# Optimization experiments

Hardware: AMD Instinct MI355X
Metric: run time of the kernel (lower is better)

The kernel has to match this reference:

```python
import jax, jax.numpy as jnp
import numpy as np

D = 1024      # embedding_dim
H = 16        # num_heads
DH = D // H   # head_dim
DFF = 4 * D
EPS = 1e-5


def setup_inputs() -> dict:
    key = jax.random.key(0)
    ks = jax.random.split(key, 10)
    B, T = 2, 2048
    s = 0.02
    return {
        "x": jax.random.normal(ks[0], (B, T, D), dtype=jnp.float32),
        "Wq": jax.random.normal(ks[1], (H, D, DH), dtype=jnp.float32) * s,
        "Wk": jax.random.normal(ks[2], (H, D, DH), dtype=jnp.float32) * s,
        "Wv": jax.random.normal(ks[3], (H, D, DH), dtype=jnp.float32) * s,
        "W1": jax.random.normal(ks[4], (D, DFF), dtype=jnp.float32) * s,
        "b1": jnp.zeros((DFF,), dtype=jnp.float32),
        "W2": jax.random.normal(ks[5], (DFF, D), dtype=jnp.float32) * s,
        "b2": jnp.zeros((D,), dtype=jnp.float32),
        "gamma1": jnp.ones((D,), dtype=jnp.float32),
        "beta1": jnp.zeros((D,), dtype=jnp.float32),
        "gamma2": jnp.ones((D,), dtype=jnp.float32),
        "beta2": jnp.zeros((D,), dtype=jnp.float32),
    }


def _layernorm(x, gamma, beta):
    # torch.var default is unbiased (ddof=1) -- faithful to LayerNorm1d
    mean = jnp.mean(x, axis=-1, keepdims=True)
    var = jnp.var(x, axis=-1, keepdims=True, ddof=1)
    return gamma * (x - mean) * jax.lax.rsqrt(var + EPS) + beta


def _block(x, Wq, Wk, Wv, W1, b1, W2, b2, gamma1, beta1, gamma2, beta2):
    B, T, _ = x.shape
    h = _layernorm(x, gamma1, beta1)
    # per-head projections stacked: [B,H,T,DH]
    Q = jnp.einsum('btd,hde->bhte', h, Wq)
    K = jnp.einsum('btd,hde->bhte', h, Wk)
    V = jnp.einsum('btd,hde->bhte', h, Wv)
    # NOTE: original scales by 1/sqrt(embedding_dim), NOT head_dim
    scores = jnp.einsum('bhqe,bhke->bhqk', Q, K) / jnp.sqrt(jnp.float32(D))
    causal = jnp.tril(jnp.ones((T, T), dtype=bool))
    scores = jnp.where(causal, scores, -jnp.inf)
    attn = jax.nn.softmax(scores, axis=-1)
    out = jnp.einsum('bhqk,bhke->bhqe', attn, V)
    # torch.cat over heads along last dim == transpose+reshape
    out = out.transpose(0, 2, 1, 3).reshape(B, T, D)
    x = x + out
    h2 = _layernorm(x, gamma2, beta2)
    ff = jax.nn.relu(h2 @ W1 + b1) @ W2 + b2  # dropout is identity at inference
    return x + ff


def reference(x, Wq, Wk, Wv, W1, b1, W2, b2, gamma1, beta1, gamma2, beta2):
    return _block(x, Wq, Wk, Wv, W1, b1, W2, b2, gamma1, beta1, gamma2, beta2)
```

## Files before the change

kernel.cpp:

```cpp
#include <hip/hip_runtime.h>

typedef unsigned short u16;
typedef __bf16 bf16;
typedef __attribute__((ext_vector_type(8))) __bf16 bf16x8;
typedef __attribute__((ext_vector_type(4))) float f32x4;
typedef __attribute__((ext_vector_type(8))) unsigned short u16x8;
typedef unsigned long long u64;

__device__ __forceinline__ float bf2f(u16 h) {
  return __uint_as_float(((unsigned int)h) << 16);
}
__device__ __forceinline__ u16 f2bf(float f) {
  unsigned int u = __float_as_uint(f);
  return (u16)((u + 0x7fffu + ((u >> 16) & 1u)) >> 16);
}
__device__ __forceinline__ u16 ld_cv(const void* p, size_t i, int f32) {
  return f32 ? f2bf(((const float*)p)[i]) : ((const u16*)p)[i];
}
__device__ __forceinline__ float ld_f(const void* p, size_t i, int f32) {
  return f32 ? ((const float*)p)[i] : bf2f(((const u16*)p)[i]);
}
__device__ __forceinline__ void async16(const u16* g, u16* l) {
  __builtin_amdgcn_global_load_lds(
      (const __attribute__((address_space(1))) unsigned int*)g,
      (__attribute__((address_space(3))) unsigned int*)l, 16, 0, 0);
}
__device__ __forceinline__ unsigned pk_bf16(float hi, float lo) {
  return __builtin_amdgcn_perm(__float_as_uint(hi) + 0x8000u,
                               __float_as_uint(lo) + 0x8000u, 0x07060302u);
}

__global__ void sniff_kernel(const u16* __restrict__ x, int* __restrict__ flag) {
  const int tid = threadIdx.x;
  int me = 0;
#pragma unroll
  for (int j = 0; j < 4; j++) {
    const u16 v = x[(tid * 4 + j) * 2];
    const int e = (v >> 7) & 0xFF;
    me = me > e ? me : e;
  }
#pragma unroll
  for (int off = 32; off > 0; off >>= 1) {
    const int o = __shfl_down(me, off);
    me = me > o ? me : o;
  }
  __shared__ int sm[4];
  if ((tid & 63) == 0) sm[tid >> 6] = me;
  __syncthreads();
  if (tid == 0) {
    int a = sm[0] > sm[1] ? sm[0] : sm[1];
    int b = sm[2] > sm[3] ? sm[2] : sm[3];
    *flag = ((a > b ? a : b) >= 140) ? 1 : 0;
  }
}

__global__ void prep_kernel(const void* __restrict__ Wq, const void* __restrict__ Wk,
                            const void* __restrict__ Wv, const void* __restrict__ W1,
                            const void* __restrict__ W2,
                            u16* __restrict__ WTq, u16* __restrict__ W1T,
                            u16* __restrict__ W2T, const int* __restrict__ flag) {
  __shared__ u16 tile[64][65];
  const int f = *flag;
  const int bid = blockIdx.x;
  const int lx = threadIdx.x & 63, ly = threadIdx.x >> 6;
  if (bid < 768) {
    const int bx = bid & 15, wh = bid >> 4;
    const int w = wh >> 4, hh = wh & 15;
    const int tr = bx * 64;
    const void* W = (w == 0) ? Wq : ((w == 1) ? Wk : Wv);
    const size_t hbase = (size_t)hh * 65536;
#pragma unroll
    for (int i = 0; i < 16; i++)
      tile[ly * 16 + i][lx] = ld_cv(W, hbase + (size_t)(tr + ly * 16 + i) * 64 + lx, f);
    __syncthreads();
#pragma unroll
    for (int i = 0; i < 16; i++)
      WTq[((size_t)(w * 1024 + hh * 64 + ly * 16 + i)) * 1024 + tr + lx] =
          tile[lx][ly * 16 + i];
  } else {
    const void* src;
    u16* dst;
    int R, C, tc, tr;
    if (bid < 1792) {
      const int j = bid - 768;
      src = W1; dst = W1T; R = 1024; C = 4096;
      tc = (j & 63) * 64; tr = (j >> 6) * 64;
    } else {
      const int j = bid - 1792;
      src = W2; dst = W2T; R = 4096; C = 1024;
      tc = (j & 15) * 64; tr = (j >> 4) * 64;
    }
#pragma unroll
    for (int i = 0; i < 16; i++)
      tile[ly * 16 + i][lx] = ld_cv(src, (size_t)(tr + ly * 16 + i) * C + tc + lx, f);
    __syncthreads();
#pragma unroll
    for (int i = 0; i < 16; i++)
      dst[(size_t)(tc + ly * 16 + i) * R + tr + lx] = tile[lx][ly * 16 + i];
  }
}

template <int EPI, int WR, int WC, bool MS>
__launch_bounds__(WR * WC * 64)
__global__ void gemm_bt(const u16* __restrict__ A, const u16* __restrict__ B,
                        int K, int KLD, int NX, int N,
                        const void* __restrict__ bias, const u16* __restrict__ res,
                        void* __restrict__ out,
                        u16* __restrict__ Qo, u16* __restrict__ Ko, u16* __restrict__ Vto,
                        const int* __restrict__ flag) {
  constexpr int BM = WR * 64, BN = WC * 64, T = WR * WC * 64;
  constexpr int RPA = T / 4;
  constexpr int RAH = BM / RPA;
  constexpr int RBH = BN / RPA;
  __shared__ __align__(16) u16 As[BM * 64];
  __shared__ __align__(16) u16 Bs[BN * 64];
  const int tid = threadIdx.x;
  const int bid = blockIdx.x;
  const int sxp = NX >> 3;
  const int xcd = bid & 7, j9 = bid >> 3;
  int m0, n0, koff = 0, khb = 0;
  if (EPI == 3) {
    m0 = (xcd * 2 + (j9 & 1)) * BM;
    n0 = ((j9 >> 1) & 7) * BN;
    khb = (j9 >> 4) & 1;
    koff = khb * K;
  } else if (MS) {
    m0 = (xcd * sxp + j9 % sxp) * BM;
    n0 = (j9 / sxp) * BN;
  } else {
    n0 = (xcd * sxp + j9 % sxp) * BN;
    m0 = (j9 / sxp) * BM;
  }
  const int wave = tid >> 6, lane = tid & 63;
  const int wm = (wave / WC) * 64, wn = (wave % WC) * 64;
  const int lm = lane & 15, lq = lane >> 4;
  const int fb = (EPI == 1 || EPI == 2) ? *flag : 0;

  const f32x4 zero = {0.f, 0.f, 0.f, 0.f};
  f32x4 acc[4][4];
#pragma unroll
  for (int i = 0; i < 4; i++)
#pragma unroll
    for (int j = 0; j < 4; j++) acc[i][j] = zero;

  const int ar = tid >> 2;
  const int ac = (tid & 3) * 8;
  const u16* Ag = A + (size_t)(m0 + ar) * KLD + koff + ac;
  const u16* Bg = B + (size_t)(n0 + ar) * KLD + koff + ac;
  u16* AsP = &As[tid * 8];
  u16* BsP = &Bs[tid * 8];

  for (int k0 = 0; k0 < K; k0 += 64) {
#pragma unroll
    for (int hh = 0; hh < 2; hh++) {
#pragma unroll
      for (int c = 0; c < RAH; c++)
        async16(Ag + k0 + hh * 32 + (size_t)c * RPA * KLD,
                AsP + hh * BM * 32 + c * RPA * 32);
#pragma unroll
      for (int c = 0; c < RBH; c++)
        async16(Bg + k0 + hh * 32 + (size_t)c * RPA * KLD,
                BsP + hh * BN * 32 + c * RPA * 32);
    }
    __syncthreads();
    bf16x8 a0[4], a1[4], b0[4], b1[4];
#pragma unroll
    for (int i = 0; i < 4; i++) {
      a0[i] = *(const bf16x8*)&As[(wm + i * 16 + lm) * 32 + lq * 8];
      a1[i] = *(const bf16x8*)&As[BM * 32 + (wm + i * 16 + lm) * 32 + lq * 8];
    }
#pragma unroll
    for (int i = 0; i < 4; i++) {
      b0[i] = *(const bf16x8*)&Bs[(wn + i * 16 + lm) * 32 + lq * 8];
      b1[i] = *(const bf16x8*)&Bs[BN * 32 + (wn + i * 16 + lm) * 32 + lq * 8];
    }
#pragma unroll
    for (int i = 0; i < 4; i++)
#pragma unroll
      for (int j = 0; j < 4; j++) {
        acc[i][j] = __builtin_amdgcn_mfma_f32_16x16x32_bf16(a0[i], b0[j], acc[i][j], 0, 0, 0);
        acc[i][j] = __builtin_amdgcn_mfma_f32_16x16x32_bf16(a1[i], b1[j], acc[i][j], 0, 0, 0);
      }
    __syncthreads();
  }

  if (EPI == 0) {
#pragma unroll
    for (int i = 0; i < 4; i++) {
      const int row0 = m0 + wm + i * 16 + lq * 4;
      const int bb = row0 >> 11, t0 = row0 & 2047;
#pragma unroll
      for (int j = 0; j < 4; j++) {
        const int col = n0 + wn + j * 16 + lm;
        const int w = col >> 10, nn = col & 1023;
        const int hh = nn >> 6, e = nn & 63;
        if (w == 2) {
          ushort4 v4;
          v4.x = f2bf(acc[i][j][0]);
          v4.y = f2bf(acc[i][j][1]);
          v4.z = f2bf(acc[i][j][2]);
          v4.w = f2bf(acc[i][j][3]);
          *(ushort4*)&Vto[(((size_t)(bb * 16 + hh)) * 64 + e) * 2048 + t0] = v4;
        } else {
          u16* dst = (w == 0) ? Qo : Ko;
#pragma unroll
          for (int r = 0; r < 4; r++)
            dst[(((size_t)(bb * 16 + hh)) * 2048 + t0 + r) * 64 + e] =
                f2bf(acc[i][j][r]);
        }
      }
    }
  } else if (EPI == 3) {
    float* P = khb ? (float*)Ko : (float*)Qo;
#pragma unroll
    for (int i = 0; i < 4; i++) {
#pragma unroll
      for (int r = 0; r < 4; r++) {
        const int row = m0 + wm + i * 16 + lq * 4 + r;
#pragma unroll
        for (int j = 0; j < 4; j++) {
          const int col = n0 + wn + j * 16 + lm;
          P[(size_t)row * N + col] = acc[i][j][r];
        }
      }
    }
  } else {
#pragma unroll
    for (int i = 0; i < 4; i++) {
#pragma unroll
      for (int r = 0; r < 4; r++) {
        const int row = m0 + wm + i * 16 + lq * 4 + r;
#pragma unroll
        for (int j = 0; j < 4; j++) {
          const int col = n0 + wn + j * 16 + lm;
          const float c = acc[i][j][r];
          if (EPI == 1) {
            const float v = c + ld_f(bias, col, fb);
            ((u16*)out)[(size_t)row * N + col] = f2bf(v > 0.f ? v : 0.f);
          } else {
            const float v = c + ld_f(bias, col, fb) + bf2f(res[(size_t)row * N + col]);
            if (fb)
              ((float*)out)[(size_t)row * N + col] = v;
            else
              ((u16*)out)[(size_t)row * N + col] = f2bf(v);
          }
        }
      }
    }
  }
}

__launch_bounds__(256)
__global__ void ffn2_reduce(const float* __restrict__ P0, const float* __restrict__ P1,
                            const void* __restrict__ bias, const u16* __restrict__ res,
                            void* __restrict__ out, const int* __restrict__ flag) {
  const int f = *flag;
  const size_t i0 = ((size_t)blockIdx.x * 256 + threadIdx.x) * 8;
  const int col = (int)(i0 & 1023);
  const float4 a0 = *(const float4*)(P0 + i0);
  const float4 a1 = *(const float4*)(P0 + i0 + 4);
  const float4 b0 = *(const float4*)(P1 + i0);
  const float4 b1 = *(const float4*)(P1 + i0 + 4);
  const u16x8 r8 = *(const u16x8*)(res + i0);
  float v[8] = {a0.x + b0.x, a0.y + b0.y, a0.z + b0.z, a0.w + b0.w,
                a1.x + b1.x, a1.y + b1.y, a1.z + b1.z, a1.w + b1.w};
#pragma unroll
  for (int k = 0; k < 8; k++) v[k] += ld_f(bias, col + k, f) + bf2f(r8[k]);
  if (f) {
    float4 o0 = {v[0], v[1], v[2], v[3]};
    float4 o1 = {v[4], v[5], v[6], v[7]};
    *(float4*)((float*)out + i0) = o0;
    *(float4*)((float*)out + i0 + 4) = o1;
  } else {
    u16x8 o8;
#pragma unroll
    for (int k = 0; k < 8; k++) o8[k] = f2bf(v[k]);
    *(u16x8*)((u16*)out + i0) = o8;
  }
}

__launch_bounds__(256)
__global__ void attn_mfma(const u16* __restrict__ Q, const u16* __restrict__ K,
                          const u16* __restrict__ Vt, const void* __restrict__ xres,
                          const int* __restrict__ flag, u16* __restrict__ x2) {
  __shared__ __align__(16) unsigned char smem[35328];
  const int tid = threadIdx.x;
  const int wave = tid >> 6, lane = tid & 63;
  const int lm = lane & 15, quad = lane >> 4;
  const int bid = blockIdx.x;
  const int xcd = bid & 7, jj = bid >> 3;
  const int bh = xcd + 8 * (jj & 3);
  const int pair = jj >> 2;
  const int b = bh >> 4, h = bh & 15;
  const int f32in = *flag;

  u16* stw = (u16*)smem + wave * 4096;
  u16* Ksw = stw;
  u16* Vsw = stw + 2048;
  float (*Olds)[32][68] = (float(*)[32][68])smem;
  float (*Llds)[2][16] = (float(*)[2][16])(smem + 34816);

  const u16* Kbh = K + (size_t)bh * 131072;
  const u16* Vbh = Vt + (size_t)bh * 131072;
  const f32x4 zero = {0.f, 0.f, 0.f, 0.f};
  const int srow = lane >> 2;
  const int schk = (lane & 3) * 8;

  union V8 { bf16x8 v; struct { u64 lo, hi; } q; };

#pragma unroll 1
  for (int phase = 0; phase < 2; phase++) {
    const int qb = phase ? (63 - pair) : pair;
    const int qw0 = qb * 32;

    bf16x8 qf[2][2];
#pragma unroll
    for (int s = 0; s < 2; s++) {
      const u16* Qp = Q + ((size_t)bh * 2048 + qw0 + s * 16 + lm) * 64 + quad * 8;
      qf[s][0] = *(const bf16x8*)Qp;
      qf[s][1] = *(const bf16x8*)(Qp + 32);
    }
    f32x4 ot[2][4];
#pragma unroll
    for (int s = 0; s < 2; s++)
#pragma unroll
      for (int j = 0; j < 4; j++) ot[s][j] = zero;
    float l[2] = {0.f, 0.f};

    const int nt = qb + 1;
    const int si = (nt * wave) >> 2;
    const int ei = (nt * (wave + 1)) >> 2;

    for (int t = si; t < ei; t++) {
      const int ks = t * 32;
#pragma unroll
      for (int hh2 = 0; hh2 < 2; hh2++)
#pragma unroll
        for (int c = 0; c < 2; c++)
          async16(Kbh + (size_t)(ks + c * 16 + srow) * 64 + hh2 * 32 + schk,
                  Ksw + hh2 * 1024 + c * 512 + lane * 8);
#pragma unroll
      for (int c = 0; c < 4; c++)
        async16(Vbh + (size_t)(c * 16 + srow) * 2048 + ks + schk,
                Vsw + c * 512 + lane * 8);
      __builtin_amdgcn_s_waitcnt(0x0F70);

      f32x4 S[2][2];
#pragma unroll
      for (int s = 0; s < 2; s++)
#pragma unroll
        for (int hh = 0; hh < 2; hh++) {
          const bf16x8 k0 = *(const bf16x8*)&Ksw[(hh * 16 + lm) * 32 + quad * 8];
          const bf16x8 k1 = *(const bf16x8*)&Ksw[1024 + (hh * 16 + lm) * 32 + quad * 8];
          f32x4 a = zero;
          a = __builtin_amdgcn_mfma_f32_16x16x32_bf16(k0, qf[s][0], a, 0, 0, 0);
          a = __builtin_amdgcn_mfma_f32_16x16x32_bf16(k1, qf[s][1], a, 0, 0, 0);
          S[s][hh] = a;
        }
      const bool maskT = (t == qb);
#pragma unroll
      for (int s = 0; s < 2; s++) {
        float p[2][4];
#pragma unroll
        for (int hh = 0; hh < 2; hh++)
#pragma unroll
          for (int r = 0; r < 4; r++) {
            float v = __expf(S[s][hh][r] * 0.03125f);
            if (maskT && (hh * 16 + quad * 4 + r > s * 16 + lm)) v = 0.f;
            l[s] += v;
            p[hh][r] = v;
          }
        unsigned pk[4];
        pk[0] = pk_bf16(p[0][1], p[0][0]);
        pk[1] = pk_bf16(p[0][3], p[0][2]);
        pk[2] = pk_bf16(p[1][1], p[1][0]);
        pk[3] = pk_bf16(p[1][3], p[1][2]);
        const bf16x8 pf = *(const bf16x8*)pk;
#pragma unroll
        for (int j = 0; j < 4; j++) {
          V8 vf;
          vf.q.lo = *(const u64*)&Vsw[(j * 16 + lm) * 32 + quad * 4];
          vf.q.hi = *(const u64*)&Vsw[(j * 16 + lm) * 32 + 16 + quad * 4];
          ot[s][j] = __builtin_amdgcn_mfma_f32_16x16x32_bf16(vf.v, pf, ot[s][j], 0, 0, 0);
        }
      }
    }

#pragma unroll
    for (int s = 0; s < 2; s++) {
      l[s] += __shfl_xor(l[s], 16);
      l[s] += __shfl_xor(l[s], 32);
    }

    __syncthreads();

#pragma unroll
    for (int s = 0; s < 2; s++)
#pragma unroll
      for (int j = 0; j < 4; j++)
        *(f32x4*)&Olds[wave][s * 16 + lm][j * 16 + quad * 4] = ot[s][j];
    if (quad == 0) {
      Llds[wave][0][lm] = l[0];
      Llds[wave][1][lm] = l[1];
    }
    __syncthreads();
    const int q = tid >> 3;
    const int e0 = (tid & 7) * 8;
    f32x4 oa = zero, ob = zero;
#pragma unroll
    for (int w = 0; w < 4; w++) {
      oa += *(const f32x4*)&Olds[w][q][e0];
      ob += *(const f32x4*)&Olds[w][q][e0 + 4];
    }
    const float lt = Llds[0][q >> 4][q & 15] + Llds[1][q >> 4][q & 15] +
                     Llds[2][q >> 4][q & 15] + Llds[3][q >> 4][q & 15];
    const float linv = 1.f / lt;
    const size_t rowbase = ((size_t)(b * 2048 + qw0 + q)) * 1024 + h * 64 + e0;
    float xv[8];
    if (f32in) {
      const float* xf = (const float*)xres + rowbase;
      const float4 u0 = *(const float4*)xf;
      const float4 u1 = *(const float4*)(xf + 4);
      xv[0] = u0.x; xv[1] = u0.y; xv[2] = u0.z; xv[3] = u0.w;
      xv[4] = u1.x; xv[5] = u1.y; xv[6] = u1.z; xv[7] = u1.w;
    } else {
      const u16x8 u = *(const u16x8*)((const u16*)xres + rowbase);
#pragma unroll
      for (int k = 0; k < 8; k++) xv[k] = bf2f(u[k]);
    }
    u16x8 o8;
#pragma unroll
    for (int k = 0; k < 4; k++) o8[k] = f2bf(xv[k] + oa[k] * linv);
#pragma unroll
    for (int k = 0; k < 4; k++) o8[4 + k] = f2bf(xv[4 + k] + ob[k] * linv);
    *(u16x8*)&x2[rowbase] = o8;
    __syncthreads();
  }
}

__launch_bounds__(256)
__global__ void ln_kernel(const void* __restrict__ x, const void* __restrict__ gamma,
                          const void* __restrict__ beta, u16* __restrict__ out,
                          const int* __restrict__ flag, int xraw) {
  const size_t row = blockIdx.x;
  const int tid = threadIdx.x;
  const int f = *flag;
  const int fx = xraw ? f : 0;
  float v0, v1, v2, v3;
  if (fx) {
    const float4 v = *((const float4*)x + row * 256 + tid);
    v0 = v.x; v1 = v.y; v2 = v.z; v3 = v.w;
  } else {
    const ushort4 u = *((const ushort4*)x + row * 256 + tid);
    v0 = bf2f(u.x); v1 = bf2f(u.y); v2 = bf2f(u.z); v3 = bf2f(u.w);
  }
  float s = v0 + v1 + v2 + v3;
  float sq = v0 * v0 + v1 * v1 + v2 * v2 + v3 * v3;
#pragma unroll
  for (int off = 32; off > 0; off >>= 1) {
    s += __shfl_down(s, off);
    sq += __shfl_down(sq, off);
  }
  __shared__ float ss[4], ssq[4];
  if ((tid & 63) == 0) { ss[tid >> 6] = s; ssq[tid >> 6] = sq; }
  __syncthreads();
  s = ss[0] + ss[1] + ss[2] + ss[3];
  sq = ssq[0] + ssq[1] + ssq[2] + ssq[3];
  const float mean = s * (1.f / 1024.f);
  const float var = (sq - 1024.f * mean * mean) * (1.f / 1023.f);
  const float rs = rsqrtf(var + 1e-5f);
  const int c0 = tid * 4;
  ushort4 o;
  o.x = f2bf(ld_f(gamma, c0 + 0, f) * (v0 - mean) * rs + ld_f(beta, c0 + 0, f));
  o.y = f2bf(ld_f(gamma, c0 + 1, f) * (v1 - mean) * rs + ld_f(beta, c0 + 1, f));
  o.z = f2bf(ld_f(gamma, c0 + 2, f) * (v2 - mean) * rs + ld_f(beta, c0 + 2, f));
  o.w = f2bf(ld_f(gamma, c0 + 3, f) * (v3 - mean) * rs + ld_f(beta, c0 + 3, f));
  *(ushort4*)&out[row * 1024 + tid * 4] = o;
}

extern "C" void kernel_launch(void* const* d_in, const int* in_sizes, int n_in,
                              void* d_out, int out_size, void* d_ws, size_t ws_size,
                              hipStream_t stream) {
  const void* x      = d_in[0];
  const void* Wq     = d_in[1];
  const void* Wk     = d_in[2];
  const void* Wv     = d_in[3];
  const void* W1     = d_in[4];
  const void* b1     = d_in[5];
  const void* W2     = d_in[6];
  const void* b2     = d_in[7];
  const void* gamma1 = d_in[8];
  const void* beta1  = d_in[9];
  const void* gamma2 = d_in[10];
  const void* beta2  = d_in[11];
  u16* ws = (u16*)d_ws;

  const size_t M4 = 4194304;
  u16* h   = ws;
  u16* Qb  = ws + 1 * M4;
  u16* Kb  = ws + 2 * M4;
  u16* Vtb = ws + 3 * M4;
  u16* WTq = ws + 4 * M4;
  u16* x2  = ws + 4 * M4;
  u16* h2  = ws + 5 * M4;
  u16* W1T = ws + 6 * M4;
  u16* W2T = ws + 7 * M4;
  u16* ff1 = ws;
  float* P0 = (float*)(ws + 1 * M4);
  float* P1 = (float*)(ws + 5 * M4);
  int* flag = (int*)(ws + 8 * M4 + 9216);

  sniff_kernel<<<1, 256, 0, stream>>>((const u16*)x, flag);
  prep_kernel<<<2816, 256, 0, stream>>>(Wq, Wk, Wv, W1, W2, WTq, W1T, W2T, flag);
  ln_kernel<<<4096, 256, 0, stream>>>(x, gamma1, beta1, h, flag, 1);
  gemm_bt<0, 4, 2, false><<<384, 512, 0, stream>>>(h, WTq, 1024, 1024, 24, 3072,
                                                   nullptr, nullptr, nullptr,
                                                   Qb, Kb, Vtb, flag);
  attn_mfma<<<1024, 256, 0, stream>>>(Qb, Kb, Vtb, x, flag, x2);
  ln_kernel<<<4096, 256, 0, stream>>>(x2, gamma2, beta2, h2, flag, 0);
  gemm_bt<1, 4, 2, false><<<512, 512, 0, stream>>>(h2, W1T, 1024, 1024, 32, 4096,
                                                   b1, nullptr, ff1,
                                                   nullptr, nullptr, nullptr, flag);
  gemm_bt<3, 4, 2, false><<<256, 512, 0, stream>>>(ff1, W2T, 2048, 4096, 8, 1024,
                                                   nullptr, nullptr, nullptr,
                                                   (u16*)P0, (u16*)P1, nullptr, flag);
  ffn2_reduce<<<2048, 256, 0, stream>>>(P0, P1, b2, x2, d_out, flag);
}
```

Before: 346.1 us.

## Store FFN2 split-K partials in bf16, shrink tile, swizzle attention LDS

FFN2 split-K partial sums are now written and read as bf16 instead of fp32, halving that intermediate traffic, and the reduce kernel is adapted to match. The FFN2 GEMM moves to a 2x2 wave tile with twice as many blocks for better occupancy. The attention K/V LDS staging uses an XOR swizzle on 16-byte chunks to cut bank conflicts on MFMA operand reads. Rounding the partials to bf16 adds some accumulation error to the output.

```diff
diff --git a/kernel.cpp b/kernel.cpp
--- a/kernel.cpp
+++ b/kernel.cpp
@@ -120,9 +120,9 @@
   const int xcd = bid & 7, j9 = bid >> 3;
   int m0, n0, koff = 0, khb = 0;
   if (EPI == 3) {
-    m0 = (xcd * 2 + (j9 & 1)) * BM;
-    n0 = ((j9 >> 1) & 7) * BN;
-    khb = (j9 >> 4) & 1;
+    m0 = (xcd * 4 + (j9 & 3)) * BM;
+    n0 = ((j9 >> 2) & 7) * BN;
+    khb = (j9 >> 5) & 1;
     koff = khb * K;
   } else if (MS) {
     m0 = (xcd * sxp + j9 % sxp) * BM;
@@ -211,7 +211,7 @@
       }
     }
   } else if (EPI == 3) {
-    float* P = khb ? (float*)Ko : (float*)Qo;
+    u16* P = khb ? Ko : Qo;
 #pragma unroll
     for (int i = 0; i < 4; i++) {
 #pragma unroll
@@ -220,7 +220,7 @@
 #pragma unroll
         for (int j = 0; j < 4; j++) {
           const int col = n0 + wn + j * 16 + lm;
-          P[(size_t)row * N + col] = acc[i][j][r];
+          P[(size_t)row * N + col] = f2bf(acc[i][j][r]);
         }
       }
     }
@@ -251,21 +251,19 @@
 }
 
 __launch_bounds__(256)
-__global__ void ffn2_reduce(const float* __restrict__ P0, const float* __restrict__ P1,
+__global__ void ffn2_reduce(const u16* __restrict__ P0, const u16* __restrict__ P1,
                             const void* __restrict__ bias, const u16* __restrict__ res,
                             void* __restrict__ out, const int* __restrict__ flag) {
   const int f = *flag;
   const size_t i0 = ((size_t)blockIdx.x * 256 + threadIdx.x) * 8;
   const int col = (int)(i0 & 1023);
-  const float4 a0 = *(const float4*)(P0 + i0);
-  const float4 a1 = *(const float4*)(P0 + i0 + 4);
-  const float4 b0 = *(const float4*)(P1 + i0);
-  const float4 b1 = *(const float4*)(P1 + i0 + 4);
+  const u16x8 a8 = *(const u16x8*)(P0 + i0);
+  const u16x8 b8 = *(const u16x8*)(P1 + i0);
   const u16x8 r8 = *(const u16x8*)(res + i0);
-  float v[8] = {a0.x + b0.x, a0.y + b0.y, a0.z + b0.z, a0.w + b0.w,
-                a1.x + b1.x, a1.y + b1.y, a1.z + b1.z, a1.w + b1.w};
-#pragma unroll
-  for (int k = 0; k < 8; k++) v[k] += ld_f(bias, col + k, f) + bf2f(r8[k]);
+  float v[8];
+#pragma unroll
+  for (int k = 0; k < 8; k++)
+    v[k] = bf2f(a8[k]) + bf2f(b8[k]) + ld_f(bias, col + k, f) + bf2f(r8[k]);
   if (f) {
     float4 o0 = {v[0], v[1], v[2], v[3]};
     float4 o1 = {v[4], v[5], v[6], v[7]};
@@ -304,7 +302,8 @@
   const u16* Vbh = Vt + (size_t)bh * 131072;
   const f32x4 zero = {0.f, 0.f, 0.f, 0.f};
   const int srow = lane >> 2;
-  const int schk = (lane & 3) * 8;
+  const int sch2 = (((lane & 3) ^ ((srow >> 1) & 3))) * 8;
+  const int rk = (lm >> 1) & 3;
 
   union V8 { bf16x8 v; struct { u64 lo, hi; } q; };
 
@@ -337,11 +336,11 @@
       for (int hh2 = 0; hh2 < 2; hh2++)
 #pragma unroll
         for (int c = 0; c < 2; c++)
-          async16(Kbh + (size_t)(ks + c * 16 + srow) * 64 + hh2 * 32 + schk,
+          async16(Kbh + (size_t)(ks + c * 16 + srow) * 64 + hh2 * 32 + sch2,
                   Ksw + hh2 * 1024 + c * 512 + lane * 8);
 #pragma unroll
       for (int c = 0; c < 4; c++)
-        async16(Vbh + (size_t)(c * 16 + srow) * 2048 + ks + schk,
+        async16(Vbh + (size_t)(c * 16 + srow) * 2048 + ks + sch2,
                 Vsw + c * 512 + lane * 8);
       __builtin_amdgcn_s_waitcnt(0x0F70);
 
@@ -350,8 +349,10 @@
       for (int s = 0; s < 2; s++)
 #pragma unroll
         for (int hh = 0; hh < 2; hh++) {
-          const bf16x8 k0 = *(const bf16x8*)&Ksw[(hh * 16 + lm) * 32 + quad * 8];
-          const bf16x8 k1 = *(const bf16x8*)&Ksw[1024 + (hh * 16 + lm) * 32 + quad * 8];
+          const bf16x8 k0 =
+              *(const bf16x8*)&Ksw[(hh * 16 + lm) * 32 + (quad ^ rk) * 8];
+          const bf16x8 k1 =
+              *(const bf16x8*)&Ksw[1024 + (hh * 16 + lm) * 32 + (quad ^ rk) * 8];
           f32x4 a = zero;
           a = __builtin_amdgcn_mfma_f32_16x16x32_bf16(k0, qf[s][0], a, 0, 0, 0);
           a = __builtin_amdgcn_mfma_f32_16x16x32_bf16(k1, qf[s][1], a, 0, 0, 0);
@@ -379,8 +380,10 @@
 #pragma unroll
         for (int j = 0; j < 4; j++) {
           V8 vf;
-          vf.q.lo = *(const u64*)&Vsw[(j * 16 + lm) * 32 + quad * 4];
-          vf.q.hi = *(const u64*)&Vsw[(j * 16 + lm) * 32 + 16 + quad * 4];
+          vf.q.lo = *(const u64*)&Vsw[(j * 16 + lm) * 32 +
+                                      (((quad >> 1)) ^ rk) * 8 + (quad & 1) * 4];
+          vf.q.hi = *(const u64*)&Vsw[(j * 16 + lm) * 32 +
+                                      (((quad >> 1) | 2) ^ rk) * 8 + (quad & 1) * 4];
           ot[s][j] = __builtin_amdgcn_mfma_f32_16x16x32_bf16(vf.v, pf, ot[s][j], 0, 0, 0);
         }
       }
@@ -506,8 +509,8 @@
   u16* W1T = ws + 6 * M4;
   u16* W2T = ws + 7 * M4;
   u16* ff1 = ws;
-  float* P0 = (float*)(ws + 1 * M4);
-  float* P1 = (float*)(ws + 5 * M4);
+  u16* P0  = ws + 5 * M4;
+  u16* P1  = ws + 6 * M4;
   int* flag = (int*)(ws + 8 * M4 + 9216);
 
   sniff_kernel<<<1, 256, 0, stream>>>((const u16*)x, flag);
@@ -521,8 +524,8 @@
   gemm_bt<1, 4, 2, false><<<512, 512, 0, stream>>>(h2, W1T, 1024, 1024, 32, 4096,
                                                    b1, nullptr, ff1,
                                                    nullptr, nullptr, nullptr, flag);
-  gemm_bt<3, 4, 2, false><<<256, 512, 0, stream>>>(ff1, W2T, 2048, 4096, 8, 1024,
+  gemm_bt<3, 2, 2, false><<<512, 256, 0, stream>>>(ff1, W2T, 2048, 4096, 8, 1024,
                                                    nullptr, nullptr, nullptr,
-                                                   (u16*)P0, (u16*)P1, nullptr, flag);
+                                                   P0, P1, nullptr, flag);
   ffn2_reduce<<<2048, 256, 0, stream>>>(P0, P1, b2, x2, d_out, flag);
 }
```

Measured after the change: 323.6 us. -6.5%, faster.
